# Kernel optimization log

Hardware: AMD Instinct MI355X
Metric: run time of the kernel (lower is better)

Reference implementation:

```python
import jax, jax.numpy as jnp
import numpy as np

HIDDEN = 4096
N_HEADS = 32
N_KV = 32
HEAD_DIM = 128
T = 2048
EPS = 1e-5
ROPE_THETA = 1000000.0


def rms_norm(x, w, eps=EPS):
    var = jnp.mean(x * x, axis=-1, keepdims=True)
    return x * jax.lax.rsqrt(var + eps) * w


def apply_rope(x, positions):
    # x: [T, H, D] ; neox-style (rotate halves), full rotary_dim = HEAD_DIM
    half = HEAD_DIM // 2
    inv_freq = 1.0 / (ROPE_THETA ** (jnp.arange(0, half, dtype=jnp.float32) / half))
    ang = positions.astype(jnp.float32)[:, None] * inv_freq  # [T, half]
    cos = jnp.cos(ang)[:, None, :]  # [T, 1, half]
    sin = jnp.sin(ang)[:, None, :]
    x1, x2 = x[..., :half], x[..., half:]
    return jnp.concatenate([x1 * cos - x2 * sin, x2 * cos + x1 * sin], axis=-1)


def setup_inputs() -> dict:
    key = jax.random.key(0)
    ks = jax.random.split(key, 5)
    s = 0.02
    qkv_out = (N_HEADS + 2 * N_KV) * HEAD_DIM
    return {
        "hidden_states": jax.random.normal(ks[0], (T, HIDDEN), jnp.float32),
        "positions": jnp.arange(T, dtype=jnp.int32),
        "w_qkv": jax.random.normal(ks[1], (qkv_out, HIDDEN), jnp.float32) * s,
        "b_qkv": jax.random.normal(ks[2], (qkv_out,), jnp.float32) * s,
        "q_norm_w": jnp.ones((N_HEADS * HEAD_DIM,), jnp.float32),
        "k_norm_w": jnp.ones((N_KV * HEAD_DIM,), jnp.float32),
        "w_o": jax.random.normal(ks[3], (HIDDEN, N_HEADS * HEAD_DIM), jnp.float32) * s,
    }


def reference(hidden_states, positions, w_qkv, b_qkv, q_norm_w, k_norm_w, w_o):
    q_size = N_HEADS * HEAD_DIM
    kv_size = N_KV * HEAD_DIM
    qkv = hidden_states @ w_qkv.T + b_qkv  # [T, q+2kv]
    q, k, v = jnp.split(qkv, [q_size, q_size + kv_size], axis=-1)
    # QK RMSNorm over the full flattened q / k widths (as in Molmo)
    q = rms_norm(q, q_norm_w)
    k = rms_norm(k, k_norm_w)
    q = apply_rope(q.reshape(T, N_HEADS, HEAD_DIM), positions)
    k = apply_rope(k.reshape(T, N_KV, HEAD_DIM), positions)
    v = v.reshape(T, N_KV, HEAD_DIM)
    scale = HEAD_DIM ** -0.5
    scores = jnp.einsum("qhd,khd->hqk", q, k) * scale  # [H, T, T]
    causal = positions[:, None] >= positions[None, :]
    scores = jnp.where(causal[None], scores, jnp.float32(-1e30))
    probs = jax.nn.softmax(scores, axis=-1)
    attn = jnp.einsum("hqk,khd->qhd", probs, v).reshape(T, N_HEADS * HEAD_DIM)
    return attn @ w_o.T
```

## Files before the change

kernel.cpp:

```cpp
#include <hip/hip_runtime.h>
#include <hip/hip_bf16.h>

#define T_SEQ 2048
#define NH 32
#define HD 128
#define QKV_N 12288
#define V_OFF 8192

typedef __bf16 bf16;
typedef __attribute__((ext_vector_type(4))) __bf16 bf16x4;
typedef __attribute__((ext_vector_type(8))) __bf16 bf16x8;
typedef __attribute__((ext_vector_type(4))) float f32x4;

#define GLDS16(g, l)                                                        \
  __builtin_amdgcn_global_load_lds(                                         \
      (const __attribute__((address_space(1))) void*)(g),                   \
      (__attribute__((address_space(3))) void*)(l), 16, 0, 0)

__device__ inline bf16x8 load8(const bf16* p) { return *(const bf16x8*)p; }
__device__ inline bf16x8 load8(const float* p) {
    f32x4 a = *(const f32x4*)p;
    f32x4 b = *(const f32x4*)(p + 4);
    bf16x8 r;
    r[0] = (bf16)a[0]; r[1] = (bf16)a[1]; r[2] = (bf16)a[2]; r[3] = (bf16)a[3];
    r[4] = (bf16)b[0]; r[5] = (bf16)b[1]; r[6] = (bf16)b[2]; r[7] = (bf16)b[3];
    return r;
}

__global__ __launch_bounds__(256)
void f32_to_bf16(const float* __restrict__ in, bf16* __restrict__ out, int n8)
{
    for (int i = blockIdx.x * 256 + threadIdx.x; i < n8; i += gridDim.x * 256)
        *(bf16x8*)(out + (size_t)i * 8) = load8(in + (size_t)i * 8);
}

#define BM 128
#define BN 128
#define BK 32

template <typename TO>
__global__ __launch_bounds__(256, 2)
void gemm_bt_glds(const bf16* __restrict__ A, int lda,
                  const bf16* __restrict__ B,
                  const float* __restrict__ bias,
                  TO* __restrict__ C, int ldc,
                  int mTiles, int colPerXcd, int K)
{
    __shared__ bf16 sA[BM * BK];
    __shared__ bf16 sB[BN * BK];
    const int tid  = threadIdx.x;
    const int wave = tid >> 6, lane = tid & 63;
    const int quad = lane >> 4, l16 = lane & 15;
    const int wm = wave >> 1, wn = wave & 1;

    int b = blockIdx.x;
    int xcd = b & 7, i = b >> 3;
    const int rowBase = (i % mTiles) * BM;
    const int colBase = (xcd * colPerXcd + i / mTiles) * BN;

    f32x4 acc[4][4] = {};

    for (int k0 = 0; k0 < K; k0 += BK) {
        __syncthreads();
        for (int r = 0; r < 2; ++r) {
            int cb = wave * 128 + r * 64;
            int c  = cb + lane;
            int row = c >> 2, kg = c & 3;
            GLDS16(A + (size_t)(rowBase + row) * lda + k0 + kg * 8, sA + cb * 8);
            GLDS16(B + (size_t)(colBase + row) * K + k0 + kg * 8, sB + cb * 8);
        }
        __syncthreads();

        bf16x8 af[4], bfr[4];
        for (int mi = 0; mi < 4; ++mi)
            af[mi] = *(const bf16x8*)(sA + (wm * 64 + mi * 16 + l16) * BK + quad * 8);
        for (int ni = 0; ni < 4; ++ni)
            bfr[ni] = *(const bf16x8*)(sB + (wn * 64 + ni * 16 + l16) * BK + quad * 8);
        for (int mi = 0; mi < 4; ++mi)
            for (int ni = 0; ni < 4; ++ni)
                acc[mi][ni] = __builtin_amdgcn_mfma_f32_16x16x32_bf16(
                    af[mi], bfr[ni], acc[mi][ni], 0, 0, 0);
    }

    for (int ni = 0; ni < 4; ++ni) {
        int col = colBase + wn * 64 + ni * 16 + l16;
        float bv = bias ? bias[col] : 0.0f;
        for (int mi = 0; mi < 4; ++mi) {
            int row0 = rowBase + wm * 64 + mi * 16 + quad * 4;
            for (int r = 0; r < 4; ++r)
                C[(size_t)(row0 + r) * ldc + col] = (TO)(acc[mi][ni][r] + bv);
        }
    }
}

template <typename TA, typename TB, typename TO>
__global__ __launch_bounds__(256, 2)
void gemm_bt_bias(const TA* __restrict__ A, int lda,
                  const TB* __restrict__ B,
                  const float* __restrict__ bias,
                  TO* __restrict__ C, int ldc,
                  int M, int N, int K)
{
    __shared__ bf16 sA[BM * BK];
    __shared__ bf16 sB[BN * BK];
    const int tid  = threadIdx.x;
    const int wave = tid >> 6, lane = tid & 63;
    const int quad = lane >> 4, l16 = lane & 15;
    const int wm = wave >> 1, wn = wave & 1;
    const int rowBase = blockIdx.x * BM;
    const int colBase = blockIdx.y * BN;

    int c0 = wave * 128 + lane;
    int rowA0 = c0 >> 2, kgA0 = c0 & 3;
    int rowA1 = (c0 + 64) >> 2, kgA1 = (c0 + 64) & 3;

    f32x4 acc[4][4] = {};

    for (int k0 = 0; k0 < K; k0 += BK) {
        bf16x8 ra0 = load8(A + (size_t)(rowBase + rowA0) * lda + k0 + kgA0 * 8);
        bf16x8 ra1 = load8(A + (size_t)(rowBase + rowA1) * lda + k0 + kgA1 * 8);
        bf16x8 rb0 = load8(B + (size_t)(colBase + rowA0) * K + k0 + kgA0 * 8);
        bf16x8 rb1 = load8(B + (size_t)(colBase + rowA1) * K + k0 + kgA1 * 8);
        __syncthreads();
        *(bf16x8*)(sA + rowA0 * BK + kgA0 * 8) = ra0;
        *(bf16x8*)(sA + rowA1 * BK + kgA1 * 8) = ra1;
        *(bf16x8*)(sB + rowA0 * BK + kgA0 * 8) = rb0;
        *(bf16x8*)(sB + rowA1 * BK + kgA1 * 8) = rb1;
        __syncthreads();

        bf16x8 af[4], bfr[4];
        for (int mi = 0; mi < 4; ++mi)
            af[mi] = *(const bf16x8*)(sA + (wm * 64 + mi * 16 + l16) * BK + quad * 8);
        for (int ni = 0; ni < 4; ++ni)
            bfr[ni] = *(const bf16x8*)(sB + (wn * 64 + ni * 16 + l16) * BK + quad * 8);
        for (int mi = 0; mi < 4; ++mi)
            for (int ni = 0; ni < 4; ++ni)
                acc[mi][ni] = __builtin_amdgcn_mfma_f32_16x16x32_bf16(
                    af[mi], bfr[ni], acc[mi][ni], 0, 0, 0);
    }

    for (int ni = 0; ni < 4; ++ni) {
        int col = colBase + wn * 64 + ni * 16 + l16;
        float bv = bias ? bias[col] : 0.0f;
        for (int mi = 0; mi < 4; ++mi) {
            int row0 = rowBase + wm * 64 + mi * 16 + quad * 4;
            for (int r = 0; r < 4; ++r)
                C[(size_t)(row0 + r) * ldc + col] = (TO)(acc[mi][ni][r] + bv);
        }
    }
}

__global__ __launch_bounds__(256)
void rmsnorm_rope(bf16* __restrict__ qkv, const float* __restrict__ qw,
                  const float* __restrict__ kw, const int* __restrict__ pos)
{
    const int t   = blockIdx.x;
    const int sel = blockIdx.y;
    bf16* x = qkv + (size_t)t * QKV_N + sel * 4096;
    const float* w = sel ? kw : qw;
    const int tid = threadIdx.x;

    float ss = 0.f;
    {
        int i0 = tid * 16;
        bf16x8 a = *(const bf16x8*)(x + i0);
        bf16x8 b = *(const bf16x8*)(x + i0 + 8);
        for (int j = 0; j < 8; ++j) { float fa = (float)a[j]; ss += fa * fa; }
        for (int j = 0; j < 8; ++j) { float fb = (float)b[j]; ss += fb * fb; }
    }
    for (int off = 1; off < 64; off <<= 1) ss += __shfl_xor(ss, off, 64);
    __shared__ float red[4];
    if ((tid & 63) == 0) red[tid >> 6] = ss;
    __syncthreads();
    float tot = red[0] + red[1] + red[2] + red[3];
    float rstd = rsqrtf(tot * (1.0f / 4096.0f) + 1e-5f);

    float fp = (float)pos[t];
    for (int i = tid; i < 2048; i += 256) {
        int h = i >> 6;
        int d = i & 63;
        int base = h * 128 + d;
        float x1 = (float)x[base]      * rstd * w[base];
        float x2 = (float)x[base + 64] * rstd * w[base + 64];
        float ang = fp * exp2f(-(float)d * 0.31143075889569023f);
        float s, c;
        sincosf(ang, &s, &c);
        x[base]      = (bf16)(x1 * c - x2 * s);
        x[base + 64] = (bf16)(x2 * c + x1 * s);
    }
}

__global__ __launch_bounds__(256)
void v_transpose(const bf16* __restrict__ qkv, bf16* __restrict__ vt)
{
    __shared__ bf16 tile[64][65];
    int t0 = blockIdx.x * 64, d0 = blockIdx.y * 64, h = blockIdx.z;
    int x = threadIdx.x & 63, y4 = threadIdx.x >> 6;
    for (int yy = y4; yy < 64; yy += 4)
        tile[yy][x] = qkv[(size_t)(t0 + yy) * QKV_N + V_OFF + h * HD + d0 + x];
    __syncthreads();
    for (int yy = y4; yy < 64; yy += 4)
        vt[(size_t)(h * HD + d0 + yy) * T_SEQ + t0 + x] = tile[x][yy];
}

#define SKP 136
#define SVP 72
#define PBP 72

__global__ __launch_bounds__(256, 2)
void flash_attn(bf16* qkv, const bf16* vt)
{
    __shared__ bf16 sK[64 * SKP];
    __shared__ bf16 sV[128 * SVP];
    __shared__ bf16 pbuf[4 * 16 * PBP];

    const int tid  = threadIdx.x;
    const int wave = tid >> 6, lane = tid & 63;
    const int quad = lane >> 4, l16 = lane & 15;
    const int h    = blockIdx.y;

    const float sc = 0.08838834764831845f * 1.4426950408889634f;
    bf16* pb = pbuf + wave * 16 * PBP;

    for (int half = 0; half < 2; ++half) {
        const int blk  = half ? (31 - (int)blockIdx.x) : (int)blockIdx.x;
        const int q0w  = blk * 64 + wave * 16;
        const int kend = blk * 64;
        const int qln  = q0w + l16;

        bf16x8 qf[4];
        {
            const bf16* qrow = qkv + (size_t)qln * QKV_N + h * HD;
            for (int c = 0; c < 4; ++c)
                qf[c] = *(const bf16x8*)(qrow + c * 32 + quad * 8);
        }

        f32x4 oacc[8] = {};
        float m2 = -1e30f, lsum = 0.f;

        for (int kb = 0; kb <= kend; kb += 64) {
            __syncthreads();
            for (int j = 0; j < 4; ++j) {
                int c = tid + j * 256;
                int r = c >> 4, off = (c & 15) * 8;
                bf16x8 v = *(const bf16x8*)(qkv + (size_t)(kb + r) * QKV_N + 4096 + h * HD + off);
                *(bf16x8*)(sK + r * SKP + off) = v;
            }
            for (int j = 0; j < 4; ++j) {
                int c = tid + j * 256;
                int d = c >> 3, off = (c & 7) * 8;
                bf16x8 v = *(const bf16x8*)(vt + (size_t)(h * HD + d) * T_SEQ + kb + off);
                *(bf16x8*)(sV + d * SVP + off) = v;
            }
            __syncthreads();

            const int stmax = (kb == kend) ? (wave + 1) : 4;

            f32x4 s[4] = {};
            for (int st = 0; st < 4; ++st) {
                if (st >= stmax) break;
                const bf16* kbase = sK + (st * 16 + l16) * SKP + quad * 8;
                for (int c = 0; c < 4; ++c) {
                    bf16x8 kf = *(const bf16x8*)(kbase + c * 32);
                    s[st] = __builtin_amdgcn_mfma_f32_16x16x32_bf16(kf, qf[c], s[st], 0, 0, 0);
                }
            }
            for (int st = 0; st < 4; ++st) {
                int k0r = kb + st * 16 + quad * 4;
                for (int r = 0; r < 4; ++r) {
                    float v = s[st][r] * sc;
                    s[st][r] = (k0r + r <= qln) ? v : -1e30f;
                }
            }
            float mx = -1e30f;
            for (int st = 0; st < 4; ++st)
                for (int r = 0; r < 4; ++r) mx = fmaxf(mx, s[st][r]);
            mx = fmaxf(mx, __shfl_xor(mx, 16, 64));
            mx = fmaxf(mx, __shfl_xor(mx, 32, 64));
            float mnew  = fmaxf(m2, mx);
            float alpha = exp2f(m2 - mnew);
            float ps = 0.f;
            for (int st = 0; st < 4; ++st)
                for (int r = 0; r < 4; ++r) {
                    float p = exp2f(s[st][r] - mnew);
                    s[st][r] = p;
                    ps += p;
                }
            ps += __shfl_xor(ps, 16, 64);
            ps += __shfl_xor(ps, 32, 64);
            lsum = lsum * alpha + ps;
            m2 = mnew;

            float ar[4];
            for (int r = 0; r < 4; ++r) ar[r] = __shfl(alpha, quad * 4 + r, 64);
            for (int c = 0; c < 8; ++c)
                for (int r = 0; r < 4; ++r) oacc[c][r] *= ar[r];

            for (int st = 0; st < 4; ++st) {
                bf16x4 pw;
                for (int r = 0; r < 4; ++r) pw[r] = (bf16)s[st][r];
                *(bf16x4*)(pb + l16 * PBP + st * 16 + quad * 4) = pw;
            }
            __builtin_amdgcn_s_waitcnt(0xC07F);
            for (int ph = 0; ph < 2; ++ph) {
                bf16x8 pf = *(const bf16x8*)(pb + l16 * PBP + ph * 32 + quad * 8);
                for (int c = 0; c < 8; ++c) {
                    bf16x8 vf = *(const bf16x8*)(sV + (c * 16 + l16) * SVP + ph * 32 + quad * 8);
                    oacc[c] = __builtin_amdgcn_mfma_f32_16x16x32_bf16(pf, vf, oacc[c], 0, 0, 0);
                }
            }
        }

        float lr[4];
        for (int r = 0; r < 4; ++r) lr[r] = __shfl(lsum, quad * 4 + r, 64);
        for (int r = 0; r < 4; ++r) {
            float inv = 1.0f / lr[r];
            int t = q0w + quad * 4 + r;
            for (int c = 0; c < 8; ++c)
                qkv[(size_t)t * QKV_N + V_OFF + h * HD + c * 16 + l16] =
                    (bf16)(oacc[c][r] * inv);
        }
    }
}

extern "C" void kernel_launch(void* const* d_in, const int* in_sizes, int n_in,
                              void* d_out, int out_size, void* d_ws, size_t ws_size,
                              hipStream_t stream)
{
    const float* hidden   = (const float*)d_in[0];
    const int*   pos      = (const int*)d_in[1];
    const float* w_qkv    = (const float*)d_in[2];
    const float* b_qkv    = (const float*)d_in[3];
    const float* q_norm_w = (const float*)d_in[4];
    const float* k_norm_w = (const float*)d_in[5];
    const float* w_o      = (const float*)d_in[6];
    float* out = (float*)d_out;

    bf16* qkv = (bf16*)d_ws;
    bf16* vt  = qkv + (size_t)T_SEQ * QKV_N;
    bf16* wqb = vt  + (size_t)4096 * T_SEQ;
    bf16* wob = wqb + (size_t)QKV_N * 4096;
    bf16* hib = wob + (size_t)4096 * 4096;
    const size_t need = ((size_t)T_SEQ * QKV_N + (size_t)4096 * T_SEQ +
                         (size_t)QKV_N * 4096 + (size_t)4096 * 4096 +
                         (size_t)T_SEQ * 4096) * 2;

    if (ws_size >= need) {
        f32_to_bf16<<<2048, 256, 0, stream>>>(hidden, hib, T_SEQ * 4096 / 8);
        f32_to_bf16<<<8192, 256, 0, stream>>>(w_qkv, wqb, QKV_N * 4096 / 8);
        f32_to_bf16<<<4096, 256, 0, stream>>>(w_o, wob, 4096 * 4096 / 8);

        gemm_bt_glds<bf16><<<8 * 16 * 12, 256, 0, stream>>>(
            hib, 4096, wqb, b_qkv, qkv, QKV_N, 16, 12, 4096);
        rmsnorm_rope<<<dim3(T_SEQ, 2), 256, 0, stream>>>(qkv, q_norm_w, k_norm_w, pos);
        v_transpose<<<dim3(T_SEQ / 64, 2, NH), 256, 0, stream>>>(qkv, vt);
        flash_attn<<<dim3(T_SEQ / 128, NH), 256, 0, stream>>>(qkv, vt);
        gemm_bt_glds<float><<<8 * 16 * 4, 256, 0, stream>>>(
            qkv + V_OFF, QKV_N, wob, nullptr, out, 4096, 16, 4, 4096);
    } else {
        gemm_bt_bias<float, float, bf16><<<dim3(T_SEQ / BM, QKV_N / BN), 256, 0, stream>>>(
            hidden, 4096, w_qkv, b_qkv, qkv, QKV_N, T_SEQ, QKV_N, 4096);
        rmsnorm_rope<<<dim3(T_SEQ, 2), 256, 0, stream>>>(qkv, q_norm_w, k_norm_w, pos);
        v_transpose<<<dim3(T_SEQ / 64, 2, NH), 256, 0, stream>>>(qkv, vt);
        flash_attn<<<dim3(T_SEQ / 128, NH), 256, 0, stream>>>(qkv, vt);
        gemm_bt_bias<bf16, float, float><<<dim3(T_SEQ / BM, 4096 / BN), 256, 0, stream>>>(
            qkv + V_OFF, QKV_N, w_o, nullptr, out, 4096, T_SEQ, 4096, 4096);
    }
}
```

Baseline: 847.3 us.

## Add 256x256-tile, 4-stage pipelined QKV GEMM kernel with 512 threads

Adds a new bf16 GEMM kernel that uses 256x256 output tiles with 8 waves, a 4-slot LDS ring filled by global_load_lds, swizzled LDS addressing, and split MFMA phases interleaved with the async loads. The QKV projection now uses this kernel instead of the 128x128 one. The aim is more operand reuse per byte loaded and better hiding of global-memory latency. In exchange it uses 128KB of LDS at one block per CU, and with 384 blocks the grid yields fewer, larger tiles, which risks poorer wave balance.

```diff
diff --git a/kernel.cpp b/kernel.cpp
--- a/kernel.cpp
+++ b/kernel.cpp
@@ -32,6 +32,135 @@
 {
     for (int i = blockIdx.x * 256 + threadIdx.x; i < n8; i += gridDim.x * 256)
         *(bf16x8*)(out + (size_t)i * 8) = load8(in + (size_t)i * 8);
+}
+
+template <typename TO>
+__global__ __launch_bounds__(512, 1)
+void gemm_bt_256(const bf16* __restrict__ A, int lda,
+                 const bf16* __restrict__ B,
+                 const float* __restrict__ bias,
+                 TO* __restrict__ C, int ldc,
+                 int mTiles, int colPerXcd, int K)
+{
+    __shared__ bf16 lds[65536];
+    bf16* ldsA = lds;
+    bf16* ldsB = lds + 32768;
+
+    const int tid  = threadIdx.x;
+    const int wave = tid >> 6, lane = tid & 63;
+    const int quad = lane >> 4, l16 = lane & 15;
+    const int wm = wave >> 2, wn = wave & 3;
+
+    const int b   = blockIdx.x;
+    const int xcd = b & 7, i = b >> 3;
+    const int rowBase = (i % mTiles) * 256;
+    const int colBase = (xcd * colPerXcd + i / mTiles) * 256;
+    const int nK = K >> 5;
+
+    const bf16* gA[2];
+    const bf16* gB[2];
+#pragma unroll
+    for (int j = 0; j < 2; ++j) {
+        int c = j * 512 + tid;
+        int d = c * 16;
+        int s = d ^ ((d >> 3) & 0x70);
+        int row = s >> 6;
+        int ke  = (s & 63) >> 1;
+        gA[j] = A + (size_t)(rowBase + row) * lda + ke;
+        gB[j] = B + (size_t)(colBase + row) * K + ke;
+    }
+
+    int offA[8], offB[4];
+#pragma unroll
+    for (int mi = 0; mi < 8; ++mi) {
+        int a = (wm * 128 + mi * 16 + l16) * 64 + quad * 16;
+        offA[mi] = (a ^ ((a >> 3) & 0x70)) >> 1;
+    }
+#pragma unroll
+    for (int ni = 0; ni < 4; ++ni) {
+        int a = (wn * 64 + ni * 16 + l16) * 64 + quad * 16;
+        offB[ni] = (a ^ ((a >> 3) & 0x70)) >> 1;
+    }
+
+    auto stageA = [&](int kt) {
+        int sl = kt & 3;
+#pragma unroll
+        for (int j = 0; j < 2; ++j)
+            GLDS16(gA[j] + kt * 32, ldsA + sl * 8192 + (j * 512 + wave * 64) * 8);
+    };
+    auto stageB = [&](int kt) {
+        int sl = kt & 3;
+#pragma unroll
+        for (int j = 0; j < 2; ++j)
+            GLDS16(gB[j] + kt * 32, ldsB + sl * 8192 + (j * 512 + wave * 64) * 8);
+    };
+
+    f32x4 acc[8][4] = {};
+
+    stageA(0); stageB(0);
+    stageA(1); stageB(1);
+    stageA(2); stageB(2);
+    asm volatile("s_waitcnt vmcnt(8)" ::: "memory");
+    __builtin_amdgcn_s_barrier();
+
+    for (int kt = 0; kt < nK; ++kt) {
+        const int sl = kt & 3;
+        const bf16* sA = ldsA + sl * 8192;
+        const bf16* sB = ldsB + sl * 8192;
+        bf16x8 af[4], bfr[4], af2[4];
+
+#pragma unroll
+        for (int mi = 0; mi < 4; ++mi) af[mi]  = *(const bf16x8*)(sA + offA[mi]);
+#pragma unroll
+        for (int ni = 0; ni < 4; ++ni) bfr[ni] = *(const bf16x8*)(sB + offB[ni]);
+        if (kt + 3 < nK) stageA(kt + 3);
+        __builtin_amdgcn_s_barrier();
+        asm volatile("s_waitcnt lgkmcnt(0)" ::: "memory");
+        __builtin_amdgcn_sched_barrier(0);
+        __builtin_amdgcn_s_setprio(1);
+#pragma unroll
+        for (int mi = 0; mi < 4; ++mi)
+#pragma unroll
+            for (int ni = 0; ni < 4; ++ni)
+                acc[mi][ni] = __builtin_amdgcn_mfma_f32_16x16x32_bf16(
+                    af[mi], bfr[ni], acc[mi][ni], 0, 0, 0);
+        __builtin_amdgcn_s_setprio(0);
+        __builtin_amdgcn_s_barrier();
+
+#pragma unroll
+        for (int mi = 0; mi < 4; ++mi) af2[mi] = *(const bf16x8*)(sA + offA[4 + mi]);
+        if (kt + 3 < nK) stageB(kt + 3);
+        __builtin_amdgcn_s_barrier();
+        asm volatile("s_waitcnt lgkmcnt(0)" ::: "memory");
+        __builtin_amdgcn_sched_barrier(0);
+        __builtin_amdgcn_s_setprio(1);
+#pragma unroll
+        for (int mi = 0; mi < 4; ++mi)
+#pragma unroll
+            for (int ni = 0; ni < 4; ++ni)
+                acc[4 + mi][ni] = __builtin_amdgcn_mfma_f32_16x16x32_bf16(
+                    af2[mi], bfr[ni], acc[4 + mi][ni], 0, 0, 0);
+        __builtin_amdgcn_s_setprio(0);
+        if (kt + 1 < nK) {
+            if (kt + 3 < nK)      asm volatile("s_waitcnt vmcnt(8)" ::: "memory");
+            else if (kt + 2 < nK) asm volatile("s_waitcnt vmcnt(4)" ::: "memory");
+            else                  asm volatile("s_waitcnt vmcnt(0)" ::: "memory");
+        }
+        __builtin_amdgcn_s_barrier();
+    }
+
+#pragma unroll
+    for (int ni = 0; ni < 4; ++ni) {
+        int col = colBase + wn * 64 + ni * 16 + l16;
+        float bv = bias ? bias[col] : 0.0f;
+#pragma unroll
+        for (int mi = 0; mi < 8; ++mi) {
+            int row0 = rowBase + wm * 128 + mi * 16 + quad * 4;
+#pragma unroll
+            for (int r = 0; r < 4; ++r)
+                C[(size_t)(row0 + r) * ldc + col] = (TO)(acc[mi][ni][r] + bv);
+        }
+    }
 }
 
 #define BM 128
@@ -350,8 +479,8 @@
         f32_to_bf16<<<8192, 256, 0, stream>>>(w_qkv, wqb, QKV_N * 4096 / 8);
         f32_to_bf16<<<4096, 256, 0, stream>>>(w_o, wob, 4096 * 4096 / 8);
 
-        gemm_bt_glds<bf16><<<8 * 16 * 12, 256, 0, stream>>>(
-            hib, 4096, wqb, b_qkv, qkv, QKV_N, 16, 12, 4096);
+        gemm_bt_256<bf16><<<8 * 8 * 6, 512, 0, stream>>>(
+            hib, 4096, wqb, b_qkv, qkv, QKV_N, 8, 6, 4096);
         rmsnorm_rope<<<dim3(T_SEQ, 2), 256, 0, stream>>>(qkv, q_norm_w, k_norm_w, pos);
         v_transpose<<<dim3(T_SEQ / 64, 2, NH), 256, 0, stream>>>(qkv, vt);
         flash_attn<<<dim3(T_SEQ / 128, NH), 256, 0, stream>>>(qkv, vt);
```

Measured after the change: 836.7 us. No clear change (-1.3%).

## Add 256x256-tile 8-phase pipelined GEMM for the QKV projection

Applied to the files above, without the earlier changes.

Adds a new GEMM kernel with 256x256 output tiles, 512 threads and 128KB of double-buffered LDS. The k-loop is split into eight phases that interleave global-to-LDS loads, LDS reads and MFMA work, using sched barriers and priority hints. The QKV projection now uses this kernel instead of the 128x128 kernel, aiming to raise data reuse per tile and hide load latency. In exchange it runs only one block per CU and launches fewer blocks (384), which may leave the grid less balanced across CUs.

```diff
diff --git a/kernel.cpp b/kernel.cpp
--- a/kernel.cpp
+++ b/kernel.cpp
@@ -32,6 +32,172 @@
 {
     for (int i = blockIdx.x * 256 + threadIdx.x; i < n8; i += gridDim.x * 256)
         *(bf16x8*)(out + (size_t)i * 8) = load8(in + (size_t)i * 8);
+}
+
+template <typename TO>
+__global__ __launch_bounds__(512, 1)
+void gemm_bt_8ph(const bf16* __restrict__ A, int lda,
+                 const bf16* __restrict__ B,
+                 const float* __restrict__ bias,
+                 TO* __restrict__ C, int ldc,
+                 int mTiles, int colPerXcd, int K)
+{
+    __shared__ char lds[131072];
+
+    const int tid  = threadIdx.x;
+    const int wave = tid >> 6, lane = tid & 63;
+    const int quad = lane >> 4, l16 = lane & 15;
+    const int wm = wave >> 2, wn = wave & 3;
+
+    const int b   = blockIdx.x;
+    const int xcd = b & 7, i = b >> 3;
+    const int rowBase = (i % mTiles) * 256;
+    const int colBase = (xcd * colPerXcd + i / mTiles) * 256;
+    const int nT  = K >> 6;
+    const int nIt = nT >> 1;
+
+    const bf16* gAs[2];
+    const bf16* gBs[2];
+#pragma unroll
+    for (int j = 0; j < 2; ++j) {
+        int d = (j * 512 + tid) * 16;
+        int s = d ^ (((d >> 7) & 7) << 4);
+        int row = s >> 7, ke = (s & 127) >> 1;
+        gAs[j] = A + (size_t)(rowBase + row) * lda + ke;
+        gBs[j] = B + (size_t)(colBase + row) * K + ke;
+    }
+
+    auto stA = [&](int kt) {
+        char* dst = (char*)lds + (kt & 1) * 32768 + wave * 1024;
+        const size_t ko = (size_t)kt * 64;
+#pragma unroll
+        for (int h = 0; h < 2; ++h)
+#pragma unroll
+            for (int j = 0; j < 2; ++j)
+                GLDS16(gAs[j] + (size_t)h * 128 * lda + ko,
+                       dst + h * 16384 + j * 8192);
+    };
+    auto stB = [&](int kt) {
+        char* dst = (char*)lds + 65536 + (kt & 1) * 32768 + wave * 1024;
+        const size_t ko = (size_t)kt * 64;
+#pragma unroll
+        for (int h = 0; h < 2; ++h)
+#pragma unroll
+            for (int j = 0; j < 2; ++j)
+                GLDS16(gBs[j] + (size_t)h * 128 * K + ko,
+                       dst + h * 16384 + j * 8192);
+    };
+
+    const int xm  = (l16 & 7) << 4;
+    const int xk0 = (quad * 16) ^ xm;
+    const int xk1 = (quad * 16 + 64) ^ xm;
+    const char* aB = (const char*)lds + wm * 16384 + l16 * 128;
+    const char* bB = (const char*)lds + 65536 + (wn >> 1) * 16384 +
+                     (wn & 1) * 8192 + l16 * 128;
+
+    f32x4 acc[8][4] = {};
+    bf16x8 aPa[4], aPb[4], bP0[4], bP1[4];
+
+#define RDA(SET, DB, MH, XK)                                                  \
+    _Pragma("unroll")                                                         \
+    for (int q_ = 0; q_ < 4; ++q_)                                            \
+        SET[q_] = *(const bf16x8*)(aB + (DB) + (MH) * 8192 + q_ * 2048 + (XK));
+
+#define RDB(SET, DB, XK)                                                      \
+    _Pragma("unroll")                                                         \
+    for (int n_ = 0; n_ < 4; ++n_)                                            \
+        SET[n_] = *(const bf16x8*)(bB + (DB) + n_ * 2048 + (XK));
+
+#define MM(MH, AS, BS)                                                        \
+    __builtin_amdgcn_s_setprio(1);                                            \
+    _Pragma("unroll")                                                         \
+    for (int q_ = 0; q_ < 4; ++q_)                                            \
+        _Pragma("unroll")                                                     \
+        for (int n_ = 0; n_ < 4; ++n_)                                        \
+            acc[(MH) * 4 + q_][n_] = __builtin_amdgcn_mfma_f32_16x16x32_bf16( \
+                AS[q_], BS[n_], acc[(MH) * 4 + q_][n_], 0, 0, 0);             \
+    __builtin_amdgcn_s_setprio(0);
+
+#define SB    __builtin_amdgcn_sched_barrier(0)
+#define BARR  __builtin_amdgcn_s_barrier()
+#define LGKM0 asm volatile("s_waitcnt lgkmcnt(0)" ::: "memory")
+
+    stB(0); stA(0); stB(1);
+    asm volatile("s_waitcnt vmcnt(4)" ::: "memory");
+    BARR;
+
+    for (int t = 0; t < nIt; ++t) {
+        const int t2 = t << 1;
+        const bool more = (t + 1 < nIt);
+
+        RDA(aPa, 0, 0, xk0); RDB(bP0, 0, xk0);
+        stA(t2 + 1);
+        SB; BARR; LGKM0; SB;
+        MM(0, aPa, bP0);
+        SB; BARR;
+
+        RDA(aPb, 0, 1, xk0);
+        SB; BARR; LGKM0; SB;
+        MM(1, aPb, bP0);
+        SB; BARR;
+
+        RDA(aPa, 0, 0, xk1); RDB(bP1, 0, xk1);
+        SB; BARR; LGKM0; SB;
+        MM(0, aPa, bP1);
+        SB; BARR;
+
+        RDA(aPb, 0, 1, xk1);
+        SB; BARR; LGKM0; SB;
+        MM(1, aPb, bP1);
+        SB;
+        asm volatile("s_waitcnt vmcnt(0)" ::: "memory");
+        BARR;
+
+        RDA(aPa, 32768, 0, xk0); RDB(bP0, 32768, xk0);
+        if (more) stB(t2 + 2);
+        SB; BARR; LGKM0; SB;
+        MM(0, aPa, bP0);
+        SB; BARR;
+
+        RDA(aPb, 32768, 1, xk0);
+        if (more) stA(t2 + 2);
+        SB; BARR; LGKM0; SB;
+        MM(1, aPb, bP0);
+        SB; BARR;
+
+        RDA(aPa, 32768, 0, xk1); RDB(bP1, 32768, xk1);
+        SB; BARR; LGKM0; SB;
+        MM(0, aPa, bP1);
+        SB; BARR;
+
+        RDA(aPb, 32768, 1, xk1);
+        if (more) stB(t2 + 3);
+        SB; BARR; LGKM0; SB;
+        MM(1, aPb, bP1);
+        SB;
+        asm volatile("s_waitcnt vmcnt(4)" ::: "memory");
+        BARR;
+    }
+
+#undef RDA
+#undef RDB
+#undef MM
+#undef SB
+#undef BARR
+#undef LGKM0
+
+#pragma unroll
+    for (int ni = 0; ni < 4; ++ni) {
+        int col = colBase + wn * 64 + ni * 16 + l16;
+        float bv = bias ? bias[col] : 0.0f;
+#pragma unroll
+        for (int mi = 0; mi < 8; ++mi) {
+            int row0 = rowBase + wm * 128 + mi * 16 + quad * 4;
+#pragma unroll
+            for (int r = 0; r < 4; ++r)
+                C[(size_t)(row0 + r) * ldc + col] = (TO)(acc[mi][ni][r] + bv);
+        }
+    }
 }
 
 #define BM 128
@@ -350,8 +516,8 @@
         f32_to_bf16<<<8192, 256, 0, stream>>>(w_qkv, wqb, QKV_N * 4096 / 8);
         f32_to_bf16<<<4096, 256, 0, stream>>>(w_o, wob, 4096 * 4096 / 8);
 
-        gemm_bt_glds<bf16><<<8 * 16 * 12, 256, 0, stream>>>(
-            hib, 4096, wqb, b_qkv, qkv, QKV_N, 16, 12, 4096);
+        gemm_bt_8ph<bf16><<<8 * 8 * 6, 512, 0, stream>>>(
+            hib, 4096, wqb, b_qkv, qkv, QKV_N, 8, 6, 4096);
         rmsnorm_rope<<<dim3(T_SEQ, 2), 256, 0, stream>>>(qkv, q_norm_w, k_norm_w, pos);
         v_transpose<<<dim3(T_SEQ / 64, 2, NH), 256, 0, stream>>>(qkv, vt);
         flash_attn<<<dim3(T_SEQ / 128, NH), 256, 0, stream>>>(qkv, vt);
```

Result: faster. 828.0 us (-2.3%).

## Pipeline GEMM with 4-stage swizzled LDS ring and 256x128 tiles

Applied to the files above, without the earlier changes.

Replaces the two-barrier-per-step bf16 GEMM with a 512-thread kernel using 256x128 output tiles. Global-to-LDS loads go into a 4-slot ring with three stages in flight, managed by explicit vmcnt waits and one barrier per K step. LDS addresses are XOR-swizzled to avoid bank conflicts, and MFMA issue gets raised priority. This hides load latency and cuts sync cost, but uses 96KB of LDS per block, which limits occupancy and grid size, and the waitcnt bookkeeping is fragile.

```diff
diff --git a/kernel.cpp b/kernel.cpp
--- a/kernel.cpp
+++ b/kernel.cpp
@@ -34,64 +34,117 @@
         *(bf16x8*)(out + (size_t)i * 8) = load8(in + (size_t)i * 8);
 }
 
-#define BM 128
-#define BN 128
-#define BK 32
-
 template <typename TO>
-__global__ __launch_bounds__(256, 2)
-void gemm_bt_glds(const bf16* __restrict__ A, int lda,
-                  const bf16* __restrict__ B,
-                  const float* __restrict__ bias,
-                  TO* __restrict__ C, int ldc,
-                  int mTiles, int colPerXcd, int K)
-{
-    __shared__ bf16 sA[BM * BK];
-    __shared__ bf16 sB[BN * BK];
+__global__ __launch_bounds__(512, 2)
+void gemm_bt_p1(const bf16* __restrict__ A, int lda,
+                const bf16* __restrict__ B,
+                const float* __restrict__ bias,
+                TO* __restrict__ C, int ldc,
+                int mTiles, int colPerXcd, int K)
+{
+    __shared__ char lds[98304];
+    char* ldsA = lds;
+    char* ldsB = lds + 65536;
+
     const int tid  = threadIdx.x;
     const int wave = tid >> 6, lane = tid & 63;
     const int quad = lane >> 4, l16 = lane & 15;
     const int wm = wave >> 1, wn = wave & 1;
 
-    int b = blockIdx.x;
-    int xcd = b & 7, i = b >> 3;
-    const int rowBase = (i % mTiles) * BM;
-    const int colBase = (xcd * colPerXcd + i / mTiles) * BN;
+    const int b   = blockIdx.x;
+    const int xcd = b & 7, i = b >> 3;
+    const int rowBase = (i % mTiles) * 256;
+    const int colBase = (xcd * colPerXcd + i / mTiles) * 128;
+    const int nK = K >> 5;
+
+    const bf16* gA0; const bf16* gA1; const bf16* gB0;
+    {
+        int d0 = tid * 16;
+        int s0 = d0 ^ ((d0 >> 3) & 0x70);
+        gA0 = A + (size_t)(rowBase + (s0 >> 6)) * lda + ((s0 & 63) >> 1);
+        int d1 = (512 + tid) * 16;
+        int s1 = d1 ^ ((d1 >> 3) & 0x70);
+        gA1 = A + (size_t)(rowBase + (s1 >> 6)) * lda + ((s1 & 63) >> 1);
+        int d2 = tid * 16;
+        int s2 = d2 ^ ((d2 >> 3) & 0x70);
+        gB0 = B + (size_t)(colBase + (s2 >> 6)) * K + ((s2 & 63) >> 1);
+    }
+
+    auto stage = [&](int kt) {
+        const int sl = kt & 3;
+        const int ko = kt * 32;
+        GLDS16(gA0 + ko, ldsA + sl * 16384 + wave * 1024);
+        GLDS16(gA1 + ko, ldsA + sl * 16384 + 8192 + wave * 1024);
+        GLDS16(gB0 + ko, ldsB + sl * 8192 + wave * 1024);
+    };
+
+    int offA[4], offB[4];
+#pragma unroll
+    for (int mi = 0; mi < 4; ++mi) {
+        int a = (wm * 64 + mi * 16 + l16) * 64 + quad * 16;
+        offA[mi] = a ^ ((a >> 3) & 0x70);
+    }
+#pragma unroll
+    for (int ni = 0; ni < 4; ++ni) {
+        int a = (wn * 64 + ni * 16 + l16) * 64 + quad * 16;
+        offB[ni] = a ^ ((a >> 3) & 0x70);
+    }
 
     f32x4 acc[4][4] = {};
 
-    for (int k0 = 0; k0 < K; k0 += BK) {
-        __syncthreads();
-        for (int r = 0; r < 2; ++r) {
-            int cb = wave * 128 + r * 64;
-            int c  = cb + lane;
-            int row = c >> 2, kg = c & 3;
-            GLDS16(A + (size_t)(rowBase + row) * lda + k0 + kg * 8, sA + cb * 8);
-            GLDS16(B + (size_t)(colBase + row) * K + k0 + kg * 8, sB + cb * 8);
-        }
-        __syncthreads();
-
+    stage(0); stage(1); stage(2);
+    asm volatile("s_waitcnt vmcnt(6)" ::: "memory");
+    __builtin_amdgcn_s_barrier();
+
+#pragma unroll 4
+    for (int kt = 0; kt < nK; ++kt) {
+        const char* sA = ldsA + (kt & 3) * 16384;
+        const char* sB = ldsB + (kt & 3) * 8192;
         bf16x8 af[4], bfr[4];
+#pragma unroll
+        for (int mi = 0; mi < 4; ++mi) af[mi]  = *(const bf16x8*)(sA + offA[mi]);
+#pragma unroll
+        for (int ni = 0; ni < 4; ++ni) bfr[ni] = *(const bf16x8*)(sB + offB[ni]);
+        if (kt + 3 < nK) stage(kt + 3);
+        __builtin_amdgcn_sched_barrier(0);
+        __builtin_amdgcn_s_setprio(1);
+#pragma unroll
         for (int mi = 0; mi < 4; ++mi)
-            af[mi] = *(const bf16x8*)(sA + (wm * 64 + mi * 16 + l16) * BK + quad * 8);
-        for (int ni = 0; ni < 4; ++ni)
-            bfr[ni] = *(const bf16x8*)(sB + (wn * 64 + ni * 16 + l16) * BK + quad * 8);
-        for (int mi = 0; mi < 4; ++mi)
+#pragma unroll
             for (int ni = 0; ni < 4; ++ni)
                 acc[mi][ni] = __builtin_amdgcn_mfma_f32_16x16x32_bf16(
                     af[mi], bfr[ni], acc[mi][ni], 0, 0, 0);
-    }
-
+        __builtin_amdgcn_s_setprio(0);
+        __builtin_amdgcn_sched_barrier(0);
+        if (kt + 3 < nK) {
+            asm volatile("s_waitcnt vmcnt(6)" ::: "memory");
+            __builtin_amdgcn_s_barrier();
+        } else if (kt + 2 < nK) {
+            asm volatile("s_waitcnt vmcnt(3)" ::: "memory");
+            __builtin_amdgcn_s_barrier();
+        } else if (kt + 1 < nK) {
+            asm volatile("s_waitcnt vmcnt(0)" ::: "memory");
+            __builtin_amdgcn_s_barrier();
+        }
+    }
+
+#pragma unroll
     for (int ni = 0; ni < 4; ++ni) {
         int col = colBase + wn * 64 + ni * 16 + l16;
         float bv = bias ? bias[col] : 0.0f;
+#pragma unroll
         for (int mi = 0; mi < 4; ++mi) {
             int row0 = rowBase + wm * 64 + mi * 16 + quad * 4;
+#pragma unroll
             for (int r = 0; r < 4; ++r)
                 C[(size_t)(row0 + r) * ldc + col] = (TO)(acc[mi][ni][r] + bv);
         }
     }
 }
+
+#define BM 128
+#define BN 128
+#define BK 32
 
 template <typename TA, typename TB, typename TO>
 __global__ __launch_bounds__(256, 2)
@@ -350,13 +403,13 @@
         f32_to_bf16<<<8192, 256, 0, stream>>>(w_qkv, wqb, QKV_N * 4096 / 8);
         f32_to_bf16<<<4096, 256, 0, stream>>>(w_o, wob, 4096 * 4096 / 8);
 
-        gemm_bt_glds<bf16><<<8 * 16 * 12, 256, 0, stream>>>(
-            hib, 4096, wqb, b_qkv, qkv, QKV_N, 16, 12, 4096);
+        gemm_bt_p1<bf16><<<768, 512, 0, stream>>>(
+            hib, 4096, wqb, b_qkv, qkv, QKV_N, 8, 12, 4096);
         rmsnorm_rope<<<dim3(T_SEQ, 2), 256, 0, stream>>>(qkv, q_norm_w, k_norm_w, pos);
         v_transpose<<<dim3(T_SEQ / 64, 2, NH), 256, 0, stream>>>(qkv, vt);
         flash_attn<<<dim3(T_SEQ / 128, NH), 256, 0, stream>>>(qkv, vt);
-        gemm_bt_glds<float><<<8 * 16 * 4, 256, 0, stream>>>(
-            qkv + V_OFF, QKV_N, wob, nullptr, out, 4096, 16, 4, 4096);
+        gemm_bt_p1<float><<<256, 512, 0, stream>>>(
+            qkv + V_OFF, QKV_N, wob, nullptr, out, 4096, 8, 4, 4096);
     } else {
         gemm_bt_bias<float, float, bf16><<<dim3(T_SEQ / BM, QKV_N / BN), 256, 0, stream>>>(
             hidden, 4096, w_qkv, b_qkv, qkv, QKV_N, T_SEQ, QKV_N, 4096);
```

Measured after the change: 798.0 us. 1.06x faster.
